# Kernel optimization log

Measured on AMD Instinct MI355X. Metric: run time of the kernel, lower is better.

Reference implementation:

```python
import jax, jax.numpy as jnp
import numpy as np

ROPE_BASE = 10000.0
NUM_HEADS = 16

def _rotate_half(x):
    d = x.shape[-1] // 2
    return jnp.concatenate([-x[..., d:], x[..., :d]], axis=-1)

def setup_inputs() -> dict:
    key = jax.random.key(0)
    ks = jax.random.split(key, 5)
    b, s, d = 1, 2048, 2048
    scale = 1.0 / np.sqrt(d)
    return {
        "hidden_states": jax.random.normal(ks[0], (b, s, d), jnp.float32),
        "wq": jax.random.normal(ks[1], (d, d), jnp.float32) * scale,
        "wk": jax.random.normal(ks[2], (d, d), jnp.float32) * scale,
        "wv": jax.random.normal(ks[3], (d, d), jnp.float32) * scale,
        "wo": jax.random.normal(ks[4], (d, d), jnp.float32) * scale,
        "position_ids": jnp.broadcast_to(jnp.arange(s, dtype=jnp.int32), (b, s)),
    }

def reference(hidden_states, wq, wk, wv, wo, position_ids):
    b, s, d = hidden_states.shape
    h = NUM_HEADS
    dh = d // h
    # q/k/v projections (torch Linear: y = x @ W^T), split heads -> bhsd
    def proj(w):
        return jnp.einsum('bsd,ed->bse', hidden_states, w).reshape(b, s, h, dh).transpose(0, 2, 1, 3)
    q, k, v = proj(wq), proj(wk), proj(wv)
    # rotary embedding (LLaMA style): freqs over half dim, duplicated
    inv_freq = 1.0 / (ROPE_BASE ** (jnp.arange(0, dh, 2, dtype=jnp.float32) / dh))
    t = jnp.arange(s, dtype=jnp.float32)
    freqs = jnp.einsum('s,f->sf', t, inv_freq)              # [s, dh/2]
    emb = jnp.concatenate([freqs, freqs], axis=-1)          # [s, dh]
    cos = jnp.cos(emb)[position_ids][:, None, :, :]         # [b,1,s,dh]
    sin = jnp.sin(emb)[position_ids][:, None, :, :]
    q = q * cos + _rotate_half(q) * sin
    k = k * cos + _rotate_half(k) * sin
    # full (non-causal) scaled dot-product attention, as in the SDPA fast path
    scores = jnp.einsum('bhqd,bhkd->bhqk', q, k) / jnp.sqrt(jnp.float32(dh))
    attn = jax.nn.softmax(scores, axis=-1)
    out = jnp.einsum('bhqk,bhkd->bhqd', attn, v)            # [b,h,s,dh]
    out = out.transpose(0, 2, 1, 3).reshape(b, s, d)
    return jnp.einsum('bsd,ed->bse', out, wo)
```

## Files before the change

kernel.cpp:

```cpp
#include <hip/hip_runtime.h>

typedef unsigned short ushort_t;
typedef unsigned int uint32;
typedef __attribute__((ext_vector_type(8))) short short8;
typedef __attribute__((ext_vector_type(4))) float f32x4;
typedef __attribute__((ext_vector_type(2))) uint32 u32x2;

#define LDS_LOAD16(gptr, lptr)                                                             \
  __builtin_amdgcn_global_load_lds((const __attribute__((address_space(1))) uint32*)(gptr),\
                                   (__attribute__((address_space(3))) uint32*)(lptr),      \
                                   16, 0, 0)

__device__ __forceinline__ ushort_t f2b(float f) {
  uint32 u = __builtin_bit_cast(uint32, f);
  u += 0x7fffu + ((u >> 16) & 1u);
  return (ushort_t)(u >> 16);
}
__device__ __forceinline__ uint32 pk2(float a, float b) {
  return (uint32)f2b(a) | ((uint32)f2b(b) << 16);
}

constexpr size_t E = (size_t)2048 * 2048;

__global__ __launch_bounds__(256) void k_cvt5(const float* __restrict__ a0, const float* __restrict__ a1,
                                              const float* __restrict__ a2, const float* __restrict__ a3,
                                              const float* __restrict__ a4, ushort_t* __restrict__ out) {
  const float* srcs[5] = {a0, a1, a2, a3, a4};
  const float* s = srcs[blockIdx.y];
  size_t i = ((size_t)blockIdx.x * 256 + threadIdx.x) * 4;
  float4 v = *(const float4*)(s + i);
  ushort4 o;
  o.x = f2b(v.x); o.y = f2b(v.y); o.z = f2b(v.z); o.w = f2b(v.w);
  *(ushort4*)(out + (size_t)blockIdx.y * E + i) = o;
}

#define SWZ3(r) (((r) >> 1) & 3)

#define STG32(srcA, srcB, dA, dB, ktile)                                        \
  do {                                                                          \
    const int koff_ = (ktile) * 32;                                             \
    _Pragma("unroll") for (int j2_ = 0; j2_ < 2; ++j2_) {                       \
      int c_ = tid + 256 * j2_;                                                 \
      int r_ = c_ >> 2, p_ = c_ & 3;                                            \
      int sc_ = (p_ ^ SWZ3(r_)) * 8;                                            \
      LDS_LOAD16((srcA) + (row0 + r_) * 2048 + koff_ + sc_, &(dA)[c_ * 8]);     \
      LDS_LOAD16((srcB) + (col0 + r_) * 2048 + koff_ + sc_, &(dB)[c_ * 8]);     \
    }                                                                           \
  } while (0)

__global__ __launch_bounds__(256, 3) void k_gemm_qkv(const ushort_t* __restrict__ A,
                                                     const ushort_t* __restrict__ B0,
                                                     const ushort_t* __restrict__ B1,
                                                     const ushort_t* __restrict__ B2,
                                                     ushort_t* __restrict__ Qm,
                                                     ushort_t* __restrict__ Km,
                                                     ushort_t* __restrict__ Vt,
                                                     const int* __restrict__ pos) {
  __shared__ ushort_t As[3][128 * 32];
  __shared__ ushort_t Bs[3][128 * 32];
  const int tid = threadIdx.x;
  const int lane = tid & 63, wave = tid >> 6;
  const int quad = lane >> 4, l16 = lane & 15;
  const int wm = wave >> 1, wn = wave & 1;
  const int z = blockIdx.z;
  const ushort_t* Bp = (z == 0) ? B0 : (z == 1) ? B1 : B2;
  const size_t row0 = (size_t)blockIdx.y * 128, col0 = (size_t)blockIdx.x * 128;

  int g[4];
#pragma unroll
  for (int j = 0; j < 4; ++j) g[j] = (j & 1) + ((j >> 1) << 2) + wn * 2;

  f32x4 zero = {0.f, 0.f, 0.f, 0.f};
  f32x4 acc[4][4];
#pragma unroll
  for (int i = 0; i < 4; ++i)
#pragma unroll
    for (int j = 0; j < 4; ++j) acc[i][j] = zero;

#define QKV_FRAGS(CUR)                                                          \
    short8 a_[4], b_[4];                                                        \
    _Pragma("unroll") for (int i_ = 0; i_ < 4; ++i_) {                          \
      int ra_ = wm * 64 + i_ * 16 + l16;                                        \
      a_[i_] = *(const short8*)&As[CUR][(ra_ * 4 + (quad ^ SWZ3(ra_))) * 8];    \
    }                                                                           \
    _Pragma("unroll") for (int j_ = 0; j_ < 4; ++j_) {                          \
      int rb_ = g[j_] * 16 + l16;                                               \
      b_[j_] = *(const short8*)&Bs[CUR][(rb_ * 4 + (quad ^ SWZ3(rb_))) * 8];    \
    }                                                                           \
    _Pragma("unroll") for (int i_ = 0; i_ < 4; ++i_)                            \
      _Pragma("unroll") for (int j_ = 0; j_ < 4; ++j_)                          \
        acc[i_][j_] = __builtin_amdgcn_mfma_f32_16x16x32_bf16(a_[i_], b_[j_], acc[i_][j_], 0, 0, 0);

#define QKV_BODY(T, CUR, STG, SEN, VM)                                          \
  do {                                                                          \
    if (SEN) STG32(A, Bp, As[STG], Bs[STG], (T) + 2);                           \
    QKV_FRAGS(CUR)                                                              \
    asm volatile("s_waitcnt " VM ::: "memory");                                 \
    __builtin_amdgcn_s_barrier();                                               \
  } while (0)

  STG32(A, Bp, As[0], Bs[0], 0);
  STG32(A, Bp, As[1], Bs[1], 1);
  asm volatile("s_waitcnt vmcnt(4)" ::: "memory");
  __builtin_amdgcn_s_barrier();

  for (int tt = 0; tt < 60; tt += 3) {
    QKV_BODY(tt + 0, 0, 2, 1, "vmcnt(4)");
    QKV_BODY(tt + 1, 1, 0, 1, "vmcnt(4)");
    QKV_BODY(tt + 2, 2, 1, 1, "vmcnt(4)");
  }
  QKV_BODY(60, 0, 2, 1, "vmcnt(4)");
  QKV_BODY(61, 1, 0, 1, "vmcnt(4)");
  QKV_BODY(62, 2, 1, 0, "vmcnt(0)");
  { QKV_FRAGS(0) }

  if (z < 2) {
    ushort_t* C = z ? Km : Qm;
    const float mul = z ? 1.0f : 0.08838834764831845f;
#pragma unroll
    for (int i = 0; i < 4; ++i)
#pragma unroll
      for (int r = 0; r < 4; ++r) {
        size_t row = row0 + wm * 64 + i * 16 + quad * 4 + r;
        float pt = (float)pos[row];
        size_t rowoff = row * 2048 + col0;
#pragma unroll
        for (int j = 0; j < 2; ++j) {
          int f = g[j] * 16 + l16;
          float ang = pt * __expf(-0.14391156831212787f * (float)f);
          float sn, cs;
          __sincosf(ang, &sn, &cs);
          cs *= mul; sn *= mul;
          float q0 = acc[i][j][r], q1 = acc[i][j + 2][r];
          C[rowoff + f]      = f2b(q0 * cs - q1 * sn);
          C[rowoff + f + 64] = f2b(q1 * cs + q0 * sn);
        }
      }
  } else {
#pragma unroll
    for (int i = 0; i < 4; ++i)
#pragma unroll
      for (int j = 0; j < 4; ++j) {
        size_t col = col0 + g[j] * 16 + l16;
        size_t rowb = row0 + wm * 64 + i * 16 + quad * 4;
        ushort4 ov;
        ov.x = f2b(acc[i][j][0]); ov.y = f2b(acc[i][j][1]);
        ov.z = f2b(acc[i][j][2]); ov.w = f2b(acc[i][j][3]);
        *(ushort4*)&Vt[col * 2048 + rowb] = ov;
      }
  }
}

__global__ __launch_bounds__(256, 2) void k_attn(const ushort_t* __restrict__ Q,
                                                 const ushort_t* __restrict__ Kg,
                                                 const ushort_t* __restrict__ Vt,
                                                 ushort_t* __restrict__ O) {
  __shared__ uint32 smem[9216 + 256 + 8192];
  ushort_t* Qs  = (ushort_t*)smem;
  uint32*   Pbf = smem + 4096;
  float*    Lred = (float*)(smem + 9216);
  ushort_t* Vs  = (ushort_t*)(smem + 9472);
  float*    Rbuf = (float*)smem;

  const int tid = threadIdx.x;
  const int lane = tid & 63, wave = tid >> 6;
  const int quad = lane >> 4, l16 = lane & 15;
  const int bid = blockIdx.x;
  const int head = ((bid & 7) << 1) + ((bid >> 3) >> 5);
  const int qt = (bid >> 3) & 31;

#pragma unroll
  for (int j = 0; j < 4; ++j) {
    int s = tid + 256 * j;
    int r = s >> 4, p = s & 15;
    LDS_LOAD16(Q + (size_t)(qt * 64 + r) * 2048 + head * 128 + ((p ^ (r & 15)) * 8), &Qs[s * 8]);
  }
  __syncthreads();

  f32x4 zero = {0.f, 0.f, 0.f, 0.f};
  f32x4 oacc[4][8];
#pragma unroll
  for (int qg = 0; qg < 4; ++qg)
#pragma unroll
    for (int ns = 0; ns < 8; ++ns) oacc[qg][ns] = zero;
  float l_acc[4] = {0.f, 0.f, 0.f, 0.f};

  const ushort_t* Kbase = Kg + (size_t)head * 128;
  const ushort_t* Vbase = Vt + (size_t)head * 128 * 2048;
  uint32* pw = Pbf + wave * 1280;
  ushort_t* Vsw = Vs + wave * 4096;
  const ushort_t* Vst = Vbase + (size_t)(lane >> 2) * 2048 + ((lane & 3) ^ ((lane >> 3) & 3)) * 8;
  const int vsw = (quad ^ ((l16 >> 1) & 3)) * 8;

  for (int it = 0; it < 16; ++it) {
    const int kb = it * 128 + wave * 32;

#pragma unroll
    for (int l = 0; l < 8; ++l)
      LDS_LOAD16(Vst + (size_t)l * 16 * 2048 + kb, &Vsw[(l * 64 + lane) * 8]);

    short8 kf[2][4];
#pragma unroll
    for (int kg = 0; kg < 2; ++kg)
#pragma unroll
      for (int kk = 0; kk < 4; ++kk)
        kf[kg][kk] = *(const short8*)&Kbase[(size_t)(kb + kg * 16 + l16) * 2048 + kk * 32 + quad * 8];

#pragma unroll
    for (int qg = 0; qg < 4; ++qg) {
      short8 qa[4];
#pragma unroll
      for (int kk = 0; kk < 4; ++kk)
        qa[kk] = *(const short8*)&Qs[((qg * 16 + l16) * 16 + ((kk * 4 + quad) ^ l16)) * 8];
      f32x4 s0 = zero, s1 = zero;
#pragma unroll
      for (int kk = 0; kk < 4; ++kk) {
        s0 = __builtin_amdgcn_mfma_f32_16x16x32_bf16(kf[0][kk], qa[kk], s0, 0, 0, 0);
        s1 = __builtin_amdgcn_mfma_f32_16x16x32_bf16(kf[1][kk], qa[kk], s1, 0, 0, 0);
      }
      float p00 = __expf(s0[0]), p01 = __expf(s0[1]);
      float p02 = __expf(s0[2]), p03 = __expf(s0[3]);
      float p10 = __expf(s1[0]), p11 = __expf(s1[1]);
      float p12 = __expf(s1[2]), p13 = __expf(s1[3]);
      l_acc[qg] += ((p00 + p01) + (p02 + p03)) + ((p10 + p11) + (p12 + p13));
      u32x2 w0, w1;
      w0[0] = pk2(p00, p01); w0[1] = pk2(p02, p03);
      w1[0] = pk2(p10, p11); w1[1] = pk2(p12, p13);
      int off = (qg * 16 + l16) * 20 + quad * 2;
      *(u32x2*)&pw[off]     = w0;
      *(u32x2*)&pw[off + 8] = w1;
    }

    short8 pb[4];
#pragma unroll
    for (int qg = 0; qg < 4; ++qg)
      pb[qg] = *(const short8*)&pw[(qg * 16 + l16) * 20 + quad * 4];

    asm volatile("s_waitcnt vmcnt(0)" ::: "memory");

#pragma unroll
    for (int ns = 0; ns < 8; ++ns) {
      const short8 vf = *(const short8*)&Vsw[(ns * 16 + l16) * 32 + vsw];
#pragma unroll
      for (int qg = 0; qg < 4; ++qg)
        oacc[qg][ns] = __builtin_amdgcn_mfma_f32_16x16x32_bf16(vf, pb[qg], oacc[qg][ns], 0, 0, 0);
    }

    asm volatile("s_waitcnt lgkmcnt(0)" ::: "memory");
  }

#pragma unroll
  for (int qg = 0; qg < 4; ++qg) {
    float l = l_acc[qg];
    l += __shfl_xor(l, 16, 64);
    l += __shfl_xor(l, 32, 64);
    l_acc[qg] = l;
  }
  if (quad == 0) {
#pragma unroll
    for (int qg = 0; qg < 4; ++qg) Lred[wave * 64 + qg * 16 + l16] = l_acc[qg];
  }

  const int tq = tid >> 4;
  const int td = (tid & 15) * 8;
  for (int qg = 0; qg < 4; ++qg) {
    __syncthreads();
#pragma unroll
    for (int ns = 0; ns < 8; ++ns)
      *(f32x4*)&Rbuf[(wave * 16 + l16) * 132 + ns * 16 + quad * 4] = oacc[qg][ns];
    __syncthreads();
    float lt = Lred[qg * 16 + tq] + Lred[64 + qg * 16 + tq] +
               Lred[128 + qg * 16 + tq] + Lred[192 + qg * 16 + tq];
    float inv = 1.0f / lt;
    f32x4 sA = zero, sB = zero;
#pragma unroll
    for (int w = 0; w < 4; ++w) {
      sA += *(const f32x4*)&Rbuf[(w * 16 + tq) * 132 + td];
      sB += *(const f32x4*)&Rbuf[(w * 16 + tq) * 132 + td + 4];
    }
    ushort4 o1, o2;
    o1.x = f2b(sA[0] * inv); o1.y = f2b(sA[1] * inv);
    o1.z = f2b(sA[2] * inv); o1.w = f2b(sA[3] * inv);
    o2.x = f2b(sB[0] * inv); o2.y = f2b(sB[1] * inv);
    o2.z = f2b(sB[2] * inv); o2.w = f2b(sB[3] * inv);
    size_t orow = (size_t)(qt * 64 + qg * 16 + tq) * 2048 + head * 128 + td;
    *(ushort4*)&O[orow] = o1;
    *(ushort4*)&O[orow + 4] = o2;
  }
}

__global__ __launch_bounds__(256, 3) void k_gemm_wo_sk(const ushort_t* __restrict__ A,
                                                       const ushort_t* __restrict__ B,
                                                       float* __restrict__ P) {
  __shared__ ushort_t As[3][128 * 32];
  __shared__ ushort_t Bs[3][128 * 32];
  const int tid = threadIdx.x;
  const int lane = tid & 63, wave = tid >> 6;
  const int quad = lane >> 4, l16 = lane & 15;
  const int wm = wave >> 1, wn = wave & 1;
  const size_t row0 = (size_t)blockIdx.y * 128, col0 = (size_t)blockIdx.x * 128;
  const int k0 = blockIdx.z * 1024;
  float* Pz = P + (size_t)blockIdx.z * E;
  const ushort_t* Ak = A + k0;
  const ushort_t* Bk = B + k0;

  f32x4 zero = {0.f, 0.f, 0.f, 0.f};
  f32x4 acc[4][4];
#pragma unroll
  for (int i = 0; i < 4; ++i)
#pragma unroll
    for (int j = 0; j < 4; ++j) acc[i][j] = zero;

#define WO_FRAGS(CUR)                                                           \
    short8 a_[4], b_[4];                                                        \
    _Pragma("unroll") for (int i_ = 0; i_ < 4; ++i_) {                          \
      int ra_ = wm * 64 + i_ * 16 + l16;                                        \
      a_[i_] = *(const short8*)&As[CUR][(ra_ * 4 + (quad ^ SWZ3(ra_))) * 8];    \
    }                                                                           \
    _Pragma("unroll") for (int j_ = 0; j_ < 4; ++j_) {                          \
      int rb_ = wn * 64 + j_ * 16 + l16;                                        \
      b_[j_] = *(const short8*)&Bs[CUR][(rb_ * 4 + (quad ^ SWZ3(rb_))) * 8];    \
    }                                                                           \
    _Pragma("unroll") for (int i_ = 0; i_ < 4; ++i_)                            \
      _Pragma("unroll") for (int j_ = 0; j_ < 4; ++j_)                          \
        acc[i_][j_] = __builtin_amdgcn_mfma_f32_16x16x32_bf16(a_[i_], b_[j_], acc[i_][j_], 0, 0, 0);

#define WO_BODY(T, CUR, STG, SEN, VM)                                           \
  do {                                                                          \
    if (SEN) STG32(Ak, Bk, As[STG], Bs[STG], (T) + 2);                          \
    WO_FRAGS(CUR)                                                               \
    asm volatile("s_waitcnt " VM ::: "memory");                                 \
    __builtin_amdgcn_s_barrier();                                               \
  } while (0)

  STG32(Ak, Bk, As[0], Bs[0], 0);
  STG32(Ak, Bk, As[1], Bs[1], 1);
  asm volatile("s_waitcnt vmcnt(4)" ::: "memory");
  __builtin_amdgcn_s_barrier();

  for (int tt = 0; tt < 27; tt += 3) {
    WO_BODY(tt + 0, 0, 2, 1, "vmcnt(4)");
    WO_BODY(tt + 1, 1, 0, 1, "vmcnt(4)");
    WO_BODY(tt + 2, 2, 1, 1, "vmcnt(4)");
  }
  WO_BODY(27, 0, 2, 1, "vmcnt(4)");
  WO_BODY(28, 1, 0, 1, "vmcnt(4)");
  WO_BODY(29, 2, 1, 1, "vmcnt(4)");
  WO_BODY(30, 0, 2, 0, "vmcnt(0)");
  { WO_FRAGS(1) }

#pragma unroll
  for (int i = 0; i < 4; ++i)
#pragma unroll
    for (int j = 0; j < 4; ++j)
#pragma unroll
      for (int r = 0; r < 4; ++r) {
        size_t row = row0 + wm * 64 + i * 16 + quad * 4 + r;
        size_t col = col0 + wn * 64 + j * 16 + l16;
        Pz[row * 2048 + col] = acc[i][j][r];
      }
}

__global__ __launch_bounds__(256) void k_red(const float* __restrict__ P, float* __restrict__ out) {
  size_t i = ((size_t)blockIdx.x * 256 + threadIdx.x) * 4;
  f32x4 a = *(const f32x4*)(P + i);
  f32x4 b = *(const f32x4*)(P + E + i);
  *(f32x4*)(out + i) = a + b;
}

extern "C" void kernel_launch(void* const* d_in, const int* in_sizes, int n_in,
                              void* d_out, int out_size, void* d_ws, size_t ws_size,
                              hipStream_t stream) {
  const float* X  = (const float*)d_in[0];
  const float* wq = (const float*)d_in[1];
  const float* wk = (const float*)d_in[2];
  const float* wv = (const float*)d_in[3];
  const float* wo = (const float*)d_in[4];
  const int*  pos = (const int*)d_in[5];
  float* out = (float*)d_out;

  if (ws_size < 9 * E * sizeof(ushort_t)) return;

  ushort_t* Xb  = (ushort_t*)d_ws;
  ushort_t* Wqb = Xb + E;
  ushort_t* Wkb = Xb + 2 * E;
  ushort_t* Wvb = Xb + 3 * E;
  ushort_t* Wob = Xb + 4 * E;
  ushort_t* Qm  = Xb + 5 * E;
  ushort_t* Km  = Xb + 6 * E;
  ushort_t* Vtm = Xb + 7 * E;
  ushort_t* Om  = Xb + 8 * E;
  float* Pf = (float*)Xb;

  dim3 b256(256);
  k_cvt5<<<dim3(4096, 5), b256, 0, stream>>>(X, wq, wk, wv, wo, Xb);
  k_gemm_qkv<<<dim3(16, 16, 3), b256, 0, stream>>>(Xb, Wqb, Wkb, Wvb, Qm, Km, Vtm, pos);
  k_attn<<<512, b256, 0, stream>>>(Qm, Km, Vtm, Om);
  k_gemm_wo_sk<<<dim3(16, 16, 2), b256, 0, stream>>>(Om, Wob, Pf);
  k_red<<<4096, b256, 0, stream>>>(Pf, out);
}
```

Baseline: 268.2 us.

## Load GEMM B fragments directly from global into registers, drop B LDS staging

Both projection GEMMs (QKV and output split-K) stop staging the weight (B) tiles through LDS. Each lane now reads its MFMA B fragments straight from global memory into double-buffered registers one k-tile ahead, while the A tile keeps its triple-buffered LDS path. The aim is to halve LDS traffic and footprint, which could allow more occupancy and fewer LDS reads per MFMA. In exchange, B global loads are narrow 16-byte per-lane reads with poorer coalescing, register pressure rises, and the vmcnt waits need careful accounting.

```diff
diff --git a/kernel.cpp b/kernel.cpp
--- a/kernel.cpp
+++ b/kernel.cpp
@@ -36,16 +36,50 @@
 
 #define SWZ3(r) (((r) >> 1) & 3)
 
-#define STG32(srcA, srcB, dA, dB, ktile)                                        \
+#define STG_A(dA, ktile)                                                        \
   do {                                                                          \
     const int koff_ = (ktile) * 32;                                             \
     _Pragma("unroll") for (int j2_ = 0; j2_ < 2; ++j2_) {                       \
       int c_ = tid + 256 * j2_;                                                 \
       int r_ = c_ >> 2, p_ = c_ & 3;                                            \
       int sc_ = (p_ ^ SWZ3(r_)) * 8;                                            \
-      LDS_LOAD16((srcA) + (row0 + r_) * 2048 + koff_ + sc_, &(dA)[c_ * 8]);     \
-      LDS_LOAD16((srcB) + (col0 + r_) * 2048 + koff_ + sc_, &(dB)[c_ * 8]);     \
+      LDS_LOAD16(Asrc + (row0 + r_) * 2048 + koff_ + sc_, &(dA)[c_ * 8]);       \
     }                                                                           \
+  } while (0)
+
+#define LOADB(dst, KT)                                                          \
+  _Pragma("unroll") for (int j_ = 0; j_ < 4; ++j_)                              \
+    (dst)[j_] = *(const short8*)(Bpt[j_] + (size_t)(KT) * 32);
+
+#define GFRAGS(ASBUF, BARR)                                                     \
+  do {                                                                          \
+    short8 a_[4];                                                               \
+    _Pragma("unroll") for (int i_ = 0; i_ < 4; ++i_) {                          \
+      int ra_ = wm * 64 + i_ * 16 + l16;                                        \
+      a_[i_] = *(const short8*)&(ASBUF)[(ra_ * 4 + (quad ^ SWZ3(ra_))) * 8];    \
+    }                                                                           \
+    _Pragma("unroll") for (int i_ = 0; i_ < 4; ++i_)                            \
+      _Pragma("unroll") for (int j_ = 0; j_ < 4; ++j_)                          \
+        acc[i_][j_] = __builtin_amdgcn_mfma_f32_16x16x32_bf16(a_[i_], (BARR)[j_], acc[i_][j_], 0, 0, 0); \
+  } while (0)
+
+#define GBODY(T, CUR, STG, BC, BN, SEN, BEN, VM)                                \
+  do {                                                                          \
+    if (BEN) { LOADB(BN, (T) + 1); }                                            \
+    if (SEN) STG_A(As[STG], (T) + 2);                                           \
+    GFRAGS(As[CUR], BC);                                                        \
+    asm volatile("s_waitcnt " VM ::: "memory");                                 \
+    __builtin_amdgcn_s_barrier();                                               \
+  } while (0)
+
+#define GPROLOGUE()                                                             \
+  do {                                                                          \
+    LOADB(b0, 0);                                                               \
+    STG_A(As[0], 0);                                                            \
+    asm volatile("" ::: "memory");                                              \
+    STG_A(As[1], 1);                                                            \
+    asm volatile("s_waitcnt vmcnt(2)" ::: "memory");                            \
+    __builtin_amdgcn_s_barrier();                                               \
   } while (0)
 
 __global__ __launch_bounds__(256, 3) void k_gemm_qkv(const ushort_t* __restrict__ A,
@@ -57,7 +91,6 @@
                                                      ushort_t* __restrict__ Vt,
                                                      const int* __restrict__ pos) {
   __shared__ ushort_t As[3][128 * 32];
-  __shared__ ushort_t Bs[3][128 * 32];
   const int tid = threadIdx.x;
   const int lane = tid & 63, wave = tid >> 6;
   const int quad = lane >> 4, l16 = lane & 15;
@@ -65,10 +98,15 @@
   const int z = blockIdx.z;
   const ushort_t* Bp = (z == 0) ? B0 : (z == 1) ? B1 : B2;
   const size_t row0 = (size_t)blockIdx.y * 128, col0 = (size_t)blockIdx.x * 128;
+  const ushort_t* Asrc = A;
 
   int g[4];
 #pragma unroll
   for (int j = 0; j < 4; ++j) g[j] = (j & 1) + ((j >> 1) << 2) + wn * 2;
+
+  const ushort_t* Bpt[4];
+#pragma unroll
+  for (int j = 0; j < 4; ++j) Bpt[j] = Bp + (size_t)(col0 + g[j] * 16 + l16) * 2048 + quad * 8;
 
   f32x4 zero = {0.f, 0.f, 0.f, 0.f};
   f32x4 acc[4][4];
@@ -77,42 +115,21 @@
 #pragma unroll
     for (int j = 0; j < 4; ++j) acc[i][j] = zero;
 
-#define QKV_FRAGS(CUR)                                                          \
-    short8 a_[4], b_[4];                                                        \
-    _Pragma("unroll") for (int i_ = 0; i_ < 4; ++i_) {                          \
-      int ra_ = wm * 64 + i_ * 16 + l16;                                        \
-      a_[i_] = *(const short8*)&As[CUR][(ra_ * 4 + (quad ^ SWZ3(ra_))) * 8];    \
-    }                                                                           \
-    _Pragma("unroll") for (int j_ = 0; j_ < 4; ++j_) {                          \
-      int rb_ = g[j_] * 16 + l16;                                               \
-      b_[j_] = *(const short8*)&Bs[CUR][(rb_ * 4 + (quad ^ SWZ3(rb_))) * 8];    \
-    }                                                                           \
-    _Pragma("unroll") for (int i_ = 0; i_ < 4; ++i_)                            \
-      _Pragma("unroll") for (int j_ = 0; j_ < 4; ++j_)                          \
-        acc[i_][j_] = __builtin_amdgcn_mfma_f32_16x16x32_bf16(a_[i_], b_[j_], acc[i_][j_], 0, 0, 0);
-
-#define QKV_BODY(T, CUR, STG, SEN, VM)                                          \
-  do {                                                                          \
-    if (SEN) STG32(A, Bp, As[STG], Bs[STG], (T) + 2);                           \
-    QKV_FRAGS(CUR)                                                              \
-    asm volatile("s_waitcnt " VM ::: "memory");                                 \
-    __builtin_amdgcn_s_barrier();                                               \
-  } while (0)
-
-  STG32(A, Bp, As[0], Bs[0], 0);
-  STG32(A, Bp, As[1], Bs[1], 1);
-  asm volatile("s_waitcnt vmcnt(4)" ::: "memory");
-  __builtin_amdgcn_s_barrier();
-
-  for (int tt = 0; tt < 60; tt += 3) {
-    QKV_BODY(tt + 0, 0, 2, 1, "vmcnt(4)");
-    QKV_BODY(tt + 1, 1, 0, 1, "vmcnt(4)");
-    QKV_BODY(tt + 2, 2, 1, 1, "vmcnt(4)");
-  }
-  QKV_BODY(60, 0, 2, 1, "vmcnt(4)");
-  QKV_BODY(61, 1, 0, 1, "vmcnt(4)");
-  QKV_BODY(62, 2, 1, 0, "vmcnt(0)");
-  { QKV_FRAGS(0) }
+  short8 b0[4], b1[4];
+  GPROLOGUE();
+
+  for (int tt = 0; tt < 60; tt += 6) {
+    GBODY(tt + 0, 0, 2, b0, b1, 1, 1, "vmcnt(6)");
+    GBODY(tt + 1, 1, 0, b1, b0, 1, 1, "vmcnt(6)");
+    GBODY(tt + 2, 2, 1, b0, b1, 1, 1, "vmcnt(6)");
+    GBODY(tt + 3, 0, 2, b1, b0, 1, 1, "vmcnt(6)");
+    GBODY(tt + 4, 1, 0, b0, b1, 1, 1, "vmcnt(6)");
+    GBODY(tt + 5, 2, 1, b1, b0, 1, 1, "vmcnt(6)");
+  }
+  GBODY(60, 0, 2, b0, b1, 1, 1, "vmcnt(6)");
+  GBODY(61, 1, 0, b1, b0, 1, 1, "vmcnt(6)");
+  GBODY(62, 2, 0, b0, b1, 0, 1, "vmcnt(4)");
+  GFRAGS(As[0], b1);
 
   if (z < 2) {
     ushort_t* C = z ? Km : Qm;
@@ -293,7 +310,6 @@
                                                        const ushort_t* __restrict__ B,
                                                        float* __restrict__ P) {
   __shared__ ushort_t As[3][128 * 32];
-  __shared__ ushort_t Bs[3][128 * 32];
   const int tid = threadIdx.x;
   const int lane = tid & 63, wave = tid >> 6;
   const int quad = lane >> 4, l16 = lane & 15;
@@ -301,8 +317,12 @@
   const size_t row0 = (size_t)blockIdx.y * 128, col0 = (size_t)blockIdx.x * 128;
   const int k0 = blockIdx.z * 1024;
   float* Pz = P + (size_t)blockIdx.z * E;
-  const ushort_t* Ak = A + k0;
-  const ushort_t* Bk = B + k0;
+  const ushort_t* Asrc = A + k0;
+
+  const ushort_t* Bpt[4];
+#pragma unroll
+  for (int j = 0; j < 4; ++j)
+    Bpt[j] = B + k0 + (size_t)(col0 + wn * 64 + j * 16 + l16) * 2048 + quad * 8;
 
   f32x4 zero = {0.f, 0.f, 0.f, 0.f};
   f32x4 acc[4][4];
@@ -311,43 +331,19 @@
 #pragma unroll
     for (int j = 0; j < 4; ++j) acc[i][j] = zero;
 
-#define WO_FRAGS(CUR)                                                           \
-    short8 a_[4], b_[4];                                                        \
-    _Pragma("unroll") for (int i_ = 0; i_ < 4; ++i_) {                          \
-      int ra_ = wm * 64 + i_ * 16 + l16;                                        \
-      a_[i_] = *(const short8*)&As[CUR][(ra_ * 4 + (quad ^ SWZ3(ra_))) * 8];    \
-    }                                                                           \
-    _Pragma("unroll") for (int j_ = 0; j_ < 4; ++j_) {                          \
-      int rb_ = wn * 64 + j_ * 16 + l16;                                        \
-      b_[j_] = *(const short8*)&Bs[CUR][(rb_ * 4 + (quad ^ SWZ3(rb_))) * 8];    \
-    }                                                                           \
-    _Pragma("unroll") for (int i_ = 0; i_ < 4; ++i_)                            \
-      _Pragma("unroll") for (int j_ = 0; j_ < 4; ++j_)                          \
-        acc[i_][j_] = __builtin_amdgcn_mfma_f32_16x16x32_bf16(a_[i_], b_[j_], acc[i_][j_], 0, 0, 0);
-
-#define WO_BODY(T, CUR, STG, SEN, VM)                                           \
-  do {                                                                          \
-    if (SEN) STG32(Ak, Bk, As[STG], Bs[STG], (T) + 2);                          \
-    WO_FRAGS(CUR)                                                               \
-    asm volatile("s_waitcnt " VM ::: "memory");                                 \
-    __builtin_amdgcn_s_barrier();                                               \
-  } while (0)
-
-  STG32(Ak, Bk, As[0], Bs[0], 0);
-  STG32(Ak, Bk, As[1], Bs[1], 1);
-  asm volatile("s_waitcnt vmcnt(4)" ::: "memory");
-  __builtin_amdgcn_s_barrier();
-
-  for (int tt = 0; tt < 27; tt += 3) {
-    WO_BODY(tt + 0, 0, 2, 1, "vmcnt(4)");
-    WO_BODY(tt + 1, 1, 0, 1, "vmcnt(4)");
-    WO_BODY(tt + 2, 2, 1, 1, "vmcnt(4)");
-  }
-  WO_BODY(27, 0, 2, 1, "vmcnt(4)");
-  WO_BODY(28, 1, 0, 1, "vmcnt(4)");
-  WO_BODY(29, 2, 1, 1, "vmcnt(4)");
-  WO_BODY(30, 0, 2, 0, "vmcnt(0)");
-  { WO_FRAGS(1) }
+  short8 b0[4], b1[4];
+  GPROLOGUE();
+
+  for (int tt = 0; tt < 30; tt += 6) {
+    GBODY(tt + 0, 0, 2, b0, b1, 1, 1, "vmcnt(6)");
+    GBODY(tt + 1, 1, 0, b1, b0, 1, 1, "vmcnt(6)");
+    GBODY(tt + 2, 2, 1, b0, b1, 1, 1, "vmcnt(6)");
+    GBODY(tt + 3, 0, 2, b1, b0, 1, 1, "vmcnt(6)");
+    GBODY(tt + 4, 1, 0, b0, b1, 1, 1, "vmcnt(6)");
+    GBODY(tt + 5, 2, 1, b1, b0, 1, 1, "vmcnt(6)");
+  }
+  GBODY(30, 0, 0, b0, b1, 0, 1, "vmcnt(4)");
+  GFRAGS(As[1], b1);
 
 #pragma unroll
   for (int i = 0; i < 4; ++i)
```

New measurement: 321.0 us. 1.2x slower.
